# Optimization experiments

Measured on AMD Instinct MI355X. Metric: run time of the kernel, lower is better.

Reference implementation:

```python
import jax, jax.numpy as jnp
import numpy as np

B, T, D = 64, 512, 256   # batch, time, input feat
H = 256                  # LSTM hidden (features)


def setup_inputs() -> dict:
    key = jax.random.key(0)
    ks = jax.random.split(key, 16)
    s = lambda k, shp, fan: jax.random.normal(k, shp, jnp.float32) / np.sqrt(fan)
    return {
        "x":  jax.random.normal(ks[0], (B, T, D), jnp.float32),
        # LSTM params: fused gates order (i, f, g, o)
        "Wi": s(ks[1], (D, 4 * H), D),
        "Wh": s(ks[2], (H, 4 * H), H),
        "b":  jnp.zeros((4 * H,), jnp.float32),
        # single-head attention (head_dim = H)
        "Wq": s(ks[3], (H, H), H), "bq": jnp.zeros((H,), jnp.float32),
        "Wk": s(ks[4], (H, H), H), "bk": jnp.zeros((H,), jnp.float32),
        "Wv": s(ks[5], (H, H), H), "bv": jnp.zeros((H,), jnp.float32),
        "Wo": s(ks[6], (H, H), H), "bo": jnp.zeros((H,), jnp.float32),
        # MLP head
        "W1": s(ks[7], (H, 32), H), "b1": jnp.zeros((32,), jnp.float32),
        "W2": s(ks[8], (32, 3), 32), "b2": jnp.zeros((3,), jnp.float32),
    }


def _lstm_scan(x, Wi, Wh, b):
    # Precompute input-to-hidden projection for all timesteps (batched GEMM)
    xg = jnp.einsum('btd,dg->btg', x, Wi) + b          # [B,T,4H]
    c0 = jnp.zeros((x.shape[0], Wh.shape[0]), x.dtype)
    h0 = jnp.zeros_like(c0)

    def step(carry, xg_t):
        c, h = carry
        g = xg_t + h @ Wh                               # [B,4H]
        i, f, gg, o = jnp.split(g, 4, axis=-1)          # flax gate order i,f,g,o
        c = jax.nn.sigmoid(f) * c + jax.nn.sigmoid(i) * jnp.tanh(gg)
        h = jax.nn.sigmoid(o) * jnp.tanh(c)
        return (c, h), h

    (_, _), hs = jax.lax.scan(step, (c0, h0), jnp.swapaxes(xg, 0, 1))
    return jnp.swapaxes(hs, 0, 1)                       # [B,T,H]


def reference(x, Wi, Wh, b, Wq, bq, Wk, bk, Wv, bv, Wo, bo, W1, b1, W2, b2):
    h = _lstm_scan(x, Wi, Wh, b)                        # [B,T,H]
    # single-head dot-product attention (self-attention)
    q = h @ Wq + bq
    k = h @ Wk + bk
    v = h @ Wv + bv
    scale = 1.0 / np.sqrt(q.shape[-1]).astype(np.float32)
    scores = jnp.einsum('bqd,bkd->bqk', q * scale, k)   # [B,T,T]
    attn = jax.nn.softmax(scores, axis=-1)
    o = jnp.einsum('bqk,bkd->bqd', attn, v)
    o = o @ Wo + bo                                     # output projection
    # head on first timestep
    z = jax.nn.relu(o[:, 0, :] @ W1 + b1)
    return z @ W2 + b2                                  # [B,3]
```

## Files before the change

### kernel.cpp

```cpp
#include <hip/hip_runtime.h>
#include <hip/hip_bf16.h>


typedef __attribute__((ext_vector_type(8))) short short8;
typedef __attribute__((ext_vector_type(4))) float float4v;

__device__ __forceinline__ unsigned short f2bf(float f) {
  unsigned u = __builtin_bit_cast(unsigned, f);
  return (unsigned short)((u + 0x7fffu + ((u >> 16) & 1u)) >> 16);
}
__device__ __forceinline__ float bf2f(unsigned short h) {
  return __builtin_bit_cast(float, ((unsigned)h) << 16);
}
__device__ __forceinline__ float bcl(unsigned u) {
  return __builtin_bit_cast(float, u << 16);
}
__device__ __forceinline__ float bch(unsigned u) {
  return __builtin_bit_cast(float, u & 0xffff0000u);
}
__device__ __forceinline__ float sigm(float x) {
  return __builtin_amdgcn_rcpf(1.f + __expf(-x));
}
__device__ __forceinline__ float tanh_f(float x) {
  return 1.f - 2.f * __builtin_amdgcn_rcpf(1.f + __expf(2.f * x));
}

__global__ void prep_all(const float* __restrict__ x,
                         const float* __restrict__ Wi,
                         const float* __restrict__ Wh,
                         unsigned short* __restrict__ xbf,
                         unsigned short* __restrict__ WiT,
                         unsigned short* __restrict__ WhP) {
  const int bid = blockIdx.x, tid = threadIdx.x;
  if (bid < 8192) {
    size_t i = ((size_t)bid * 256 + tid) * 4;
    float4 v = *(const float4*)&x[i];
    unsigned long long pk = (unsigned long long)f2bf(v.x)
                          | ((unsigned long long)f2bf(v.y) << 16)
                          | ((unsigned long long)f2bf(v.z) << 32)
                          | ((unsigned long long)f2bf(v.w) << 48);
    *(unsigned long long*)&xbf[i] = pk;
  } else if (bid < 8448) {
    size_t i = ((size_t)(bid - 8192) * 256 + tid) * 4;
    float4 v = *(const float4*)&Wi[i];
    int k = (int)(i >> 10), n = (int)(i & 1023);
    WiT[(size_t)(n + 0) * 256 + k] = f2bf(v.x);
    WiT[(size_t)(n + 1) * 256 + k] = f2bf(v.y);
    WiT[(size_t)(n + 2) * 256 + k] = f2bf(v.z);
    WiT[(size_t)(n + 3) * 256 + k] = f2bf(v.w);
  } else {
    size_t i0 = ((size_t)(bid - 8448) * 256 + tid) * 4;
    int row = (int)(i0 >> 8);
    int colnat = (row & 3) * 256 + (row >> 7) * 32 + ((row >> 4) & 7) * 4 +
                 ((row >> 2) & 3);
    unsigned long long pk = 0;
#pragma unroll
    for (int j = 0; j < 4; ++j) {
      int k = (int)((i0 + j) & 255);
      pk |= (unsigned long long)f2bf(Wh[(size_t)k * 1024 + colnat]) << (16 * j);
    }
    *(unsigned long long*)&WhP[i0] = pk;
  }
}

#define XKP 40
__global__ __launch_bounds__(256) void xg_gemm(const unsigned short* __restrict__ xbf,
                                               const unsigned short* __restrict__ WiT,
                                               const float* __restrict__ bias,
                                               unsigned short* __restrict__ xg) {
  __shared__ unsigned short As[128 * XKP];
  __shared__ unsigned short Bs[128 * XKP];
  const int tid = threadIdx.x;
  const int n0 = blockIdx.x * 128, m0 = blockIdx.y * 128;
  const int wave = tid >> 6, lane = tid & 63, quad = lane >> 4, l16 = lane & 15;
  const int wm = wave >> 1, wn = wave & 1;

  float4v acc[4][4];
#pragma unroll
  for (int i = 0; i < 4; ++i)
#pragma unroll
    for (int j = 0; j < 4; ++j) acc[i][j] = (float4v){0.f, 0.f, 0.f, 0.f};

  const int rr = tid >> 2, c8 = (tid & 3) * 8;
  for (int k0 = 0; k0 < 256; k0 += 32) {
#pragma unroll
    for (int pp = 0; pp < 2; ++pp) {
      int r = pp * 64 + rr;
      *(uint4*)&As[r * XKP + c8] = *(const uint4*)&xbf[(size_t)(m0 + r) * 256 + k0 + c8];
      *(uint4*)&Bs[r * XKP + c8] = *(const uint4*)&WiT[(size_t)(n0 + r) * 256 + k0 + c8];
    }
    __syncthreads();
#pragma unroll
    for (int mt = 0; mt < 4; ++mt) {
      short8 af = *(const short8*)&As[(wm * 64 + mt * 16 + l16) * XKP + quad * 8];
#pragma unroll
      for (int nt = 0; nt < 4; ++nt) {
        short8 bf = *(const short8*)&Bs[(wn * 64 + nt * 16 + l16) * XKP + quad * 8];
        acc[mt][nt] = __builtin_amdgcn_mfma_f32_16x16x32_bf16(af, bf, acc[mt][nt], 0, 0, 0);
      }
    }
    __syncthreads();
  }
#pragma unroll
  for (int nt = 0; nt < 4; ++nt) {
    int col = n0 + wn * 64 + nt * 16 + l16;
    int gate = col >> 8, u = col & 255;
    float bv = bias[col];
#pragma unroll
    for (int mt = 0; mt < 4; ++mt) {
#pragma unroll
      for (int r = 0; r < 4; ++r) {
        int row = m0 + wm * 64 + mt * 16 + quad * 4 + r;
        int b = row >> 9, t = row & 511;
        xg[(((size_t)b * 512 + t) * 256 + u) * 4 + gate] = f2bf(acc[mt][nt][r] + bv);
      }
    }
  }
}

__global__ __launch_bounds__(512, 2) void lstm_scan(
    const unsigned short* __restrict__ WhP,
    const unsigned short* __restrict__ xg,
    unsigned short* __restrict__ hout) {
  __shared__ unsigned short WhL[16 * 4096];
  __shared__ unsigned short hA[2][256];
  const int tid = threadIdx.x;
  const int b = blockIdx.x;
  const int wave = tid >> 6, lane = tid & 63, quad = lane >> 4, l16 = lane & 15;

  short8 frA[3][8];
#pragma unroll
  for (int rt = 0; rt < 3; ++rt) {
    const unsigned short* src =
        WhP + ((size_t)wave * 128 + rt * 16 + l16) * 256 + quad * 8;
#pragma unroll
    for (int kt = 0; kt < 8; ++kt)
      frA[rt][kt] = *(const short8*)&src[kt * 32];
  }
#pragma unroll
  for (int i = 0; i < 16; ++i) {
    int rt = 3 + (i >> 3);
    int chunk = (i & 7) * 64 + lane;
    int rw = chunk >> 5, ch = chunk & 31;
    uint4 v = *(const uint4*)&WhP[((size_t)wave * 128 + rt * 16 + rw) * 256 + ch * 8];
    *(uint4*)((char*)WhL + (wave * 2 + rt - 3) * 8192 + rw * 512 +
              ((ch * 16) ^ ((rw & 7) << 4))) = v;
  }
  ((unsigned short*)hA)[tid] = 0;
  __syncthreads();

  const bool act = (l16 < 8);
  const int u = wave * 32 + l16 * 4 + quad;
  const unsigned short* xgp = xg + ((size_t)b * 512 * 256 + u) * 4;
  unsigned short* houtp = hout + (size_t)b * 512 * 256 + u;
  const char* ldsT = (const char*)WhL + wave * 2 * 8192 + l16 * 512;
  const unsigned short* sp5 = WhP + ((size_t)wave * 128 + 5 * 16 + l16) * 256 + quad * 8;
  const unsigned short* sp6 = WhP + ((size_t)wave * 128 + 6 * 16 + l16) * 256 + quad * 8;
  const unsigned short* sp7 = WhP + ((size_t)wave * 128 + 7 * 16 + l16) * 256 + quad * 8;
  float c = 0.f;

  for (int t = 0; t < 512; ++t) {
    short8 sb[8];
#pragma unroll
    for (int kt = 0; kt < 8; ++kt) sb[kt] = *(const short8*)&sp5[kt * 32];

    unsigned long long xv = 0;
    if (act) xv = *(const unsigned long long*)(xgp + (size_t)t * 1024);

    const char* hbuf = (const char*)hA[t & 1];
    short8 hb8[8];
#pragma unroll
    for (int kt = 0; kt < 8; ++kt)
      hb8[kt] = *(const short8*)(hbuf + kt * 64 + quad * 16);

    float4v g4 = (float4v){0.f, 0.f, 0.f, 0.f};

#pragma unroll
    for (int p = 0; p < 3; ++p) {
      float4v a = (float4v){0.f, 0.f, 0.f, 0.f};
#pragma unroll
      for (int kt = 0; kt < 8; ++kt)
        a = __builtin_amdgcn_mfma_f32_16x16x32_bf16(frA[p][kt], hb8[kt], a, 0, 0, 0);
      if (l16 == p) g4 = a;
    }

    short8 sc[8];
#pragma unroll
    for (int kt = 0; kt < 8; ++kt) sc[kt] = *(const short8*)&sp6[kt * 32];

#pragma unroll
    for (int p = 0; p < 2; ++p) {
      float4v a = (float4v){0.f, 0.f, 0.f, 0.f};
#pragma unroll
      for (int kt = 0; kt < 8; ++kt) {
        short8 al = *(const short8*)(ldsT + p * 8192 +
                                     ((kt * 64 + quad * 16) ^ ((l16 & 7) << 4)));
        a = __builtin_amdgcn_mfma_f32_16x16x32_bf16(al, hb8[kt], a, 0, 0, 0);
      }
      if (l16 == 3 + p) g4 = a;
    }

    {
      float4v a = (float4v){0.f, 0.f, 0.f, 0.f};
#pragma unroll
      for (int kt = 0; kt < 8; ++kt)
        a = __builtin_amdgcn_mfma_f32_16x16x32_bf16(sb[kt], hb8[kt], a, 0, 0, 0);
      if (l16 == 5) g4 = a;
    }
#pragma unroll
    for (int kt = 0; kt < 8; ++kt) sb[kt] = *(const short8*)&sp7[kt * 32];

    {
      float4v a = (float4v){0.f, 0.f, 0.f, 0.f};
#pragma unroll
      for (int kt = 0; kt < 8; ++kt)
        a = __builtin_amdgcn_mfma_f32_16x16x32_bf16(sc[kt], hb8[kt], a, 0, 0, 0);
      if (l16 == 6) g4 = a;
    }
    {
      float4v a = (float4v){0.f, 0.f, 0.f, 0.f};
#pragma unroll
      for (int kt = 0; kt < 8; ++kt)
        a = __builtin_amdgcn_mfma_f32_16x16x32_bf16(sb[kt], hb8[kt], a, 0, 0, 0);
      if (l16 == 7) g4 = a;
    }

    if (act) {
      float gi = g4[0] + bf2f((unsigned short)(xv));
      float gf = g4[1] + bf2f((unsigned short)(xv >> 16));
      float gG = g4[2] + bf2f((unsigned short)(xv >> 32));
      float go = g4[3] + bf2f((unsigned short)(xv >> 48));
      float cc = sigm(gf) * c + sigm(gi) * tanh_f(gG);
      c = cc;
      unsigned short h16 = f2bf(sigm(go) * tanh_f(cc));
      hA[(t + 1) & 1][u] = h16;
      houtp[(size_t)t * 256] = h16;
    }
    __syncthreads();
  }
}

__global__ __launch_bounds__(256) void attn_head(
    const unsigned short* __restrict__ hout,
    const float* __restrict__ Wq, const float* __restrict__ bq,
    const float* __restrict__ Wk, const float* __restrict__ bk,
    const float* __restrict__ Wv, const float* __restrict__ bv,
    const float* __restrict__ Wo, const float* __restrict__ bo,
    const float* __restrict__ W1, const float* __restrict__ b1,
    const float* __restrict__ W2, const float* __restrict__ b2,
    float* __restrict__ out) {
  __shared__ float h0S[256], q0S[256], red[256], usS[256], sS[512], hb4[4][256];
  __shared__ float oS[256], o1S[256], zS[32], cbS;
  const int b = blockIdx.x, tid = threadIdx.x, wave = tid >> 6, lane = tid & 63;
  const size_t hb_base = (size_t)b * 512 * 256;

  h0S[tid] = bf2f(hout[hb_base + tid]);
  __syncthreads();
  float a = 0.f;
  for (int k = 0; k < 256; ++k) a += h0S[k] * Wq[(size_t)k * 256 + tid];
  q0S[tid] = a + bq[tid];
  __syncthreads();
  red[tid] = q0S[tid] * bk[tid];
  __syncthreads();
  for (int s = 128; s > 0; s >>= 1) {
    if (tid < s) red[tid] += red[tid + s];
    __syncthreads();
  }
  if (tid == 0) cbS = 0.0625f * red[0];
  float acq = 0.f;
  const float* wr = &Wk[(size_t)tid * 256];
  for (int e = 0; e < 256; e += 4) {
    float4 w = *(const float4*)&wr[e];
    acq += w.x * q0S[e] + w.y * q0S[e + 1] + w.z * q0S[e + 2] + w.w * q0S[e + 3];
  }
  usS[tid] = 0.0625f * acq;
  __syncthreads();

  const float u0 = usS[lane * 4 + 0], u1 = usS[lane * 4 + 1];
  const float u2 = usS[lane * 4 + 2], u3 = usS[lane * 4 + 3];
  const float cbv = cbS;
  for (int i = 0; i < 128; ++i) {
    int t = i * 4 + wave;
    unsigned long long hv = *(const unsigned long long*)&hout[hb_base + (size_t)t * 256 + lane * 4];
    unsigned lo = (unsigned)hv, hi = (unsigned)(hv >> 32);
    float p = u0 * bcl(lo) + u1 * bch(lo) + u2 * bcl(hi) + u3 * bch(hi);
    for (int m = 1; m < 64; m <<= 1) p += __shfl_xor(p, m, 64);
    if (lane == 0) sS[t] = p + cbv;
  }
  __syncthreads();
  red[tid] = fmaxf(sS[tid], sS[tid + 256]);
  __syncthreads();
  for (int s = 128; s > 0; s >>= 1) {
    if (tid < s) red[tid] = fmaxf(red[tid], red[tid + s]);
    __syncthreads();
  }
  float mx = red[0];
  __syncthreads();
  float e0 = __expf(sS[tid] - mx), e1 = __expf(sS[tid + 256] - mx);
  sS[tid] = e0; sS[tid + 256] = e1;
  red[tid] = e0 + e1;
  __syncthreads();
  for (int s = 128; s > 0; s >>= 1) {
    if (tid < s) red[tid] += red[tid + s];
    __syncthreads();
  }
  float inv = 1.f / red[0];
  float a0 = 0.f, a1 = 0.f, a2 = 0.f, a3 = 0.f;
  const int d0 = lane * 4;
  for (int i = 0; i < 128; ++i) {
    int t = wave * 128 + i;
    float w = sS[t];
    unsigned long long hv = *(const unsigned long long*)&hout[hb_base + (size_t)t * 256 + d0];
    unsigned lo = (unsigned)hv, hi = (unsigned)(hv >> 32);
    a0 += w * bcl(lo); a1 += w * bch(lo); a2 += w * bcl(hi); a3 += w * bch(hi);
  }
  hb4[wave][d0] = a0; hb4[wave][d0 + 1] = a1; hb4[wave][d0 + 2] = a2; hb4[wave][d0 + 3] = a3;
  __syncthreads();
  h0S[tid] = (hb4[0][tid] + hb4[1][tid] + hb4[2][tid] + hb4[3][tid]) * inv;
  __syncthreads();

  a = 0.f;
  for (int k = 0; k < 256; ++k) a += h0S[k] * Wv[(size_t)k * 256 + tid];
  oS[tid] = a + bv[tid];
  __syncthreads();
  a = 0.f;
  for (int k = 0; k < 256; ++k) a += oS[k] * Wo[(size_t)k * 256 + tid];
  o1S[tid] = a + bo[tid];
  __syncthreads();
  if (tid < 32) {
    a = 0.f;
    for (int k = 0; k < 256; ++k) a += o1S[k] * W1[k * 32 + tid];
    zS[tid] = fmaxf(a + b1[tid], 0.f);
  }
  __syncthreads();
  if (tid < 3) {
    a = 0.f;
    for (int j = 0; j < 32; ++j) a += zS[j] * W2[j * 3 + tid];
    out[b * 3 + tid] = a + b2[tid];
  }
}

extern "C" void kernel_launch(void* const* d_in, const int* in_sizes, int n_in,
                              void* d_out, int out_size, void* d_ws, size_t ws_size,
                              hipStream_t stream) {
  const float* x  = (const float*)d_in[0];
  const float* Wi = (const float*)d_in[1];
  const float* Wh = (const float*)d_in[2];
  const float* bG = (const float*)d_in[3];
  const float* Wq = (const float*)d_in[4];
  const float* bq = (const float*)d_in[5];
  const float* Wk = (const float*)d_in[6];
  const float* bk = (const float*)d_in[7];
  const float* Wv = (const float*)d_in[8];
  const float* bv = (const float*)d_in[9];
  const float* Wo = (const float*)d_in[10];
  const float* bo = (const float*)d_in[11];
  const float* W1 = (const float*)d_in[12];
  const float* b1 = (const float*)d_in[13];
  const float* W2 = (const float*)d_in[14];
  const float* b2 = (const float*)d_in[15];
  float* out = (float*)d_out;
  char* ws = (char*)d_ws;

  unsigned short* xg   = (unsigned short*)(ws);
  unsigned short* hout = (unsigned short*)(ws + 67108864);
  unsigned short* xbf  = (unsigned short*)(ws + 83886080);
  unsigned short* WiT  = (unsigned short*)(ws + 100663296);
  unsigned short* WhP  = (unsigned short*)(ws + 101187584);

  prep_all<<<dim3(8704), dim3(256), 0, stream>>>(x, Wi, Wh, xbf, WiT, WhP);
  xg_gemm<<<dim3(8, 256), dim3(256), 0, stream>>>(xbf, WiT, bG, xg);
  lstm_scan<<<dim3(64), dim3(512), 0, stream>>>(WhP, xg, hout);
  attn_head<<<dim3(64), dim3(256), 0, stream>>>(hout, Wq, bq, Wk, bk, Wv, bv,
                                                Wo, bo, W1, b1, W2, b2, out);
}
```

Measured before the change: 1.161 ms.

## Rebalance LSTM Wh tiles across registers, LDS and streamed global loads per wave

Changes how the 8 per-wave 16-row tiles of the recurrent weight are split between resident registers (now 4), LDS (19 slots, 2-3 per wave) and per-step global reloads (1-2 per wave), with wave-dependent counts. The first streamed tile is prefetched at the end of the previous step so it overlaps the barrier. Occupancy is pinned via waves_per_eu. The goal is to cut per-timestep global/L2 traffic on the serial recurrence critical path. The cost is higher register pressure, a larger LDS footprint, and wave divergence in loop trip counts.

New measurement: 1.551 ms. 1.34x slower.

```diff
diff --git a/kernel.cpp b/kernel.cpp
--- a/kernel.cpp
+++ b/kernel.cpp
@@ -118,52 +118,57 @@
   }
 }
 
-__global__ __launch_bounds__(512, 2) void lstm_scan(
-    const unsigned short* __restrict__ WhP,
-    const unsigned short* __restrict__ xg,
-    unsigned short* __restrict__ hout) {
-  __shared__ unsigned short WhL[16 * 4096];
+__global__ __launch_bounds__(512)
+__attribute__((amdgpu_waves_per_eu(2, 2)))
+void lstm_scan(const unsigned short* __restrict__ WhP,
+               const unsigned short* __restrict__ xg,
+               unsigned short* __restrict__ hout) {
+  __shared__ unsigned short WhL[19 * 4096];
   __shared__ unsigned short hA[2][256];
   const int tid = threadIdx.x;
   const int b = blockIdx.x;
-  const int wave = tid >> 6, lane = tid & 63, quad = lane >> 4, l16 = lane & 15;
-
-  short8 frA[3][8];
-#pragma unroll
-  for (int rt = 0; rt < 3; ++rt) {
+  const int wave = __builtin_amdgcn_readfirstlane(tid >> 6);
+  const int lane = tid & 63, quad = lane >> 4, l16 = lane & 15;
+  const int nS = (wave < 3) ? 1 : 2;
+  const int nL = 4 - nS;
+  const int slotBase = (wave < 3) ? wave * 3 : 9 + (wave - 3) * 2;
+
+  short8 frA[4][8];
+#pragma unroll
+  for (int j = 0; j < 4; ++j) {
     const unsigned short* src =
-        WhP + ((size_t)wave * 128 + rt * 16 + l16) * 256 + quad * 8;
+        WhP + ((size_t)wave * 128 + (nS + j) * 16 + l16) * 256 + quad * 8;
 #pragma unroll
     for (int kt = 0; kt < 8; ++kt)
-      frA[rt][kt] = *(const short8*)&src[kt * 32];
-  }
-#pragma unroll
-  for (int i = 0; i < 16; ++i) {
-    int rt = 3 + (i >> 3);
-    int chunk = (i & 7) * 64 + lane;
-    int rw = chunk >> 5, ch = chunk & 31;
-    uint4 v = *(const uint4*)&WhP[((size_t)wave * 128 + rt * 16 + rw) * 256 + ch * 8];
-    *(uint4*)((char*)WhL + (wave * 2 + rt - 3) * 8192 + rw * 512 +
-              ((ch * 16) ^ ((rw & 7) << 4))) = v;
+      frA[j][kt] = *(const short8*)&src[kt * 32];
+  }
+  for (int j = 0; j < nL; ++j) {
+    int rt = nS + 4 + j;
+    for (int i = 0; i < 8; ++i) {
+      int chunk = i * 64 + lane;
+      int rw = chunk >> 5, ch = chunk & 31;
+      uint4 v = *(const uint4*)&WhP[((size_t)wave * 128 + rt * 16 + rw) * 256 + ch * 8];
+      *(uint4*)((char*)WhL + (slotBase + j) * 8192 + rw * 512 +
+                ((ch * 16) ^ ((rw & 7) << 4))) = v;
+    }
   }
   ((unsigned short*)hA)[tid] = 0;
-  __syncthreads();
 
   const bool act = (l16 < 8);
   const int u = wave * 32 + l16 * 4 + quad;
   const unsigned short* xgp = xg + ((size_t)b * 512 * 256 + u) * 4;
   unsigned short* houtp = hout + (size_t)b * 512 * 256 + u;
-  const char* ldsT = (const char*)WhL + wave * 2 * 8192 + l16 * 512;
-  const unsigned short* sp5 = WhP + ((size_t)wave * 128 + 5 * 16 + l16) * 256 + quad * 8;
-  const unsigned short* sp6 = WhP + ((size_t)wave * 128 + 6 * 16 + l16) * 256 + quad * 8;
-  const unsigned short* sp7 = WhP + ((size_t)wave * 128 + 7 * 16 + l16) * 256 + quad * 8;
+  const char* ldsT = (const char*)WhL + slotBase * 8192 + l16 * 512;
+  const unsigned short* sp0 = WhP + ((size_t)wave * 128 + 0 * 16 + l16) * 256 + quad * 8;
+  const unsigned short* sp1 = WhP + ((size_t)wave * 128 + 1 * 16 + l16) * 256 + quad * 8;
   float c = 0.f;
 
+  short8 sb[8];
+#pragma unroll
+  for (int kt = 0; kt < 8; ++kt) sb[kt] = *(const short8*)&sp0[kt * 32];
+  __syncthreads();
+
   for (int t = 0; t < 512; ++t) {
-    short8 sb[8];
-#pragma unroll
-    for (int kt = 0; kt < 8; ++kt) sb[kt] = *(const short8*)&sp5[kt * 32];
-
     unsigned long long xv = 0;
     if (act) xv = *(const unsigned long long*)(xgp + (size_t)t * 1024);
 
@@ -175,54 +180,39 @@
 
     float4v g4 = (float4v){0.f, 0.f, 0.f, 0.f};
 
-#pragma unroll
-    for (int p = 0; p < 3; ++p) {
+    {
       float4v a = (float4v){0.f, 0.f, 0.f, 0.f};
 #pragma unroll
       for (int kt = 0; kt < 8; ++kt)
-        a = __builtin_amdgcn_mfma_f32_16x16x32_bf16(frA[p][kt], hb8[kt], a, 0, 0, 0);
-      if (l16 == p) g4 = a;
-    }
-
-    short8 sc[8];
-#pragma unroll
-    for (int kt = 0; kt < 8; ++kt) sc[kt] = *(const short8*)&sp6[kt * 32];
-
-#pragma unroll
-    for (int p = 0; p < 2; ++p) {
+        a = __builtin_amdgcn_mfma_f32_16x16x32_bf16(sb[kt], hb8[kt], a, 0, 0, 0);
+      if (l16 == 0) g4 = a;
+    }
+    if (nS == 2) {
+#pragma unroll
+      for (int kt = 0; kt < 8; ++kt) sb[kt] = *(const short8*)&sp1[kt * 32];
       float4v a = (float4v){0.f, 0.f, 0.f, 0.f};
 #pragma unroll
+      for (int kt = 0; kt < 8; ++kt)
+        a = __builtin_amdgcn_mfma_f32_16x16x32_bf16(sb[kt], hb8[kt], a, 0, 0, 0);
+      if (l16 == 1) g4 = a;
+    }
+#pragma unroll
+    for (int j = 0; j < 4; ++j) {
+      float4v a = (float4v){0.f, 0.f, 0.f, 0.f};
+#pragma unroll
+      for (int kt = 0; kt < 8; ++kt)
+        a = __builtin_amdgcn_mfma_f32_16x16x32_bf16(frA[j][kt], hb8[kt], a, 0, 0, 0);
+      if (l16 == nS + j) g4 = a;
+    }
+    for (int j = 0; j < nL; ++j) {
+      float4v a = (float4v){0.f, 0.f, 0.f, 0.f};
+#pragma unroll
       for (int kt = 0; kt < 8; ++kt) {
-        short8 al = *(const short8*)(ldsT + p * 8192 +
+        short8 al = *(const short8*)(ldsT + j * 8192 +
                                      ((kt * 64 + quad * 16) ^ ((l16 & 7) << 4)));
         a = __builtin_amdgcn_mfma_f32_16x16x32_bf16(al, hb8[kt], a, 0, 0, 0);
       }
-      if (l16 == 3 + p) g4 = a;
-    }
-
-    {
-      float4v a = (float4v){0.f, 0.f, 0.f, 0.f};
-#pragma unroll
-      for (int kt = 0; kt < 8; ++kt)
-        a = __builtin_amdgcn_mfma_f32_16x16x32_bf16(sb[kt], hb8[kt], a, 0, 0, 0);
-      if (l16 == 5) g4 = a;
-    }
-#pragma unroll
-    for (int kt = 0; kt < 8; ++kt) sb[kt] = *(const short8*)&sp7[kt * 32];
-
-    {
-      float4v a = (float4v){0.f, 0.f, 0.f, 0.f};
-#pragma unroll
-      for (int kt = 0; kt < 8; ++kt)
-        a = __builtin_amdgcn_mfma_f32_16x16x32_bf16(sc[kt], hb8[kt], a, 0, 0, 0);
-      if (l16 == 6) g4 = a;
-    }
-    {
-      float4v a = (float4v){0.f, 0.f, 0.f, 0.f};
-#pragma unroll
-      for (int kt = 0; kt < 8; ++kt)
-        a = __builtin_amdgcn_mfma_f32_16x16x32_bf16(sb[kt], hb8[kt], a, 0, 0, 0);
-      if (l16 == 7) g4 = a;
+      if (l16 == nS + 4 + j) g4 = a;
     }
 
     if (act) {
@@ -236,6 +226,8 @@
       hA[(t + 1) & 1][u] = h16;
       houtp[(size_t)t * 256] = h16;
     }
+#pragma unroll
+    for (int kt = 0; kt < 8; ++kt) sb[kt] = *(const short8*)&sp0[kt * 32];
     __syncthreads();
   }
 }
```

## Stream Wh tiles from global through a rotating double-buffered register pipeline

Applied to the files above, without the earlier changes.

Stops keeping three Wh row tiles resident in registers. Six row tiles are now streamed from global/L2 every timestep through a two-slot register double buffer, each load issued one tile ahead of its use. LDS still holds two tiles, now tiles 6-7 instead of 3-4, and the launch-bounds minimum-blocks hint is dropped. This frees VGPRs and overlaps weight loads with MFMA work, but it adds more global loads on each serial recurrence step.

Measured after the change: 1.627 ms. 40.1% more time.

```diff
diff --git a/kernel.cpp b/kernel.cpp
--- a/kernel.cpp
+++ b/kernel.cpp
@@ -118,7 +118,7 @@
   }
 }
 
-__global__ __launch_bounds__(512, 2) void lstm_scan(
+__global__ __launch_bounds__(512) void lstm_scan(
     const unsigned short* __restrict__ WhP,
     const unsigned short* __restrict__ xg,
     unsigned short* __restrict__ hout) {
@@ -128,42 +128,33 @@
   const int b = blockIdx.x;
   const int wave = tid >> 6, lane = tid & 63, quad = lane >> 4, l16 = lane & 15;
 
-  short8 frA[3][8];
-#pragma unroll
-  for (int rt = 0; rt < 3; ++rt) {
-    const unsigned short* src =
-        WhP + ((size_t)wave * 128 + rt * 16 + l16) * 256 + quad * 8;
-#pragma unroll
-    for (int kt = 0; kt < 8; ++kt)
-      frA[rt][kt] = *(const short8*)&src[kt * 32];
-  }
 #pragma unroll
   for (int i = 0; i < 16; ++i) {
-    int rt = 3 + (i >> 3);
+    int rt = 6 + (i >> 3);
     int chunk = (i & 7) * 64 + lane;
     int rw = chunk >> 5, ch = chunk & 31;
     uint4 v = *(const uint4*)&WhP[((size_t)wave * 128 + rt * 16 + rw) * 256 + ch * 8];
-    *(uint4*)((char*)WhL + (wave * 2 + rt - 3) * 8192 + rw * 512 +
+    *(uint4*)((char*)WhL + (wave * 2 + rt - 6) * 8192 + rw * 512 +
               ((ch * 16) ^ ((rw & 7) << 4))) = v;
   }
   ((unsigned short*)hA)[tid] = 0;
-  __syncthreads();
 
   const bool act = (l16 < 8);
   const int u = wave * 32 + l16 * 4 + quad;
   const unsigned short* xgp = xg + ((size_t)b * 512 * 256 + u) * 4;
   unsigned short* houtp = hout + (size_t)b * 512 * 256 + u;
   const char* ldsT = (const char*)WhL + wave * 2 * 8192 + l16 * 512;
-  const unsigned short* sp5 = WhP + ((size_t)wave * 128 + 5 * 16 + l16) * 256 + quad * 8;
-  const unsigned short* sp6 = WhP + ((size_t)wave * 128 + 6 * 16 + l16) * 256 + quad * 8;
-  const unsigned short* sp7 = WhP + ((size_t)wave * 128 + 7 * 16 + l16) * 256 + quad * 8;
+  const unsigned short* sp = WhP + ((size_t)wave * 128 + l16) * 256 + quad * 8;
   float c = 0.f;
 
+  short8 buf[2][8];
+#pragma unroll
+  for (int kt = 0; kt < 8; ++kt) buf[0][kt] = *(const short8*)&sp[0 * 4096 + kt * 32];
+#pragma unroll
+  for (int kt = 0; kt < 8; ++kt) buf[1][kt] = *(const short8*)&sp[1 * 4096 + kt * 32];
+  __syncthreads();
+
   for (int t = 0; t < 512; ++t) {
-    short8 sb[8];
-#pragma unroll
-    for (int kt = 0; kt < 8; ++kt) sb[kt] = *(const short8*)&sp5[kt * 32];
-
     unsigned long long xv = 0;
     if (act) xv = *(const unsigned long long*)(xgp + (size_t)t * 1024);
 
@@ -176,17 +167,17 @@
     float4v g4 = (float4v){0.f, 0.f, 0.f, 0.f};
 
 #pragma unroll
-    for (int p = 0; p < 3; ++p) {
+    for (int p = 0; p < 6; ++p) {
       float4v a = (float4v){0.f, 0.f, 0.f, 0.f};
 #pragma unroll
       for (int kt = 0; kt < 8; ++kt)
-        a = __builtin_amdgcn_mfma_f32_16x16x32_bf16(frA[p][kt], hb8[kt], a, 0, 0, 0);
+        a = __builtin_amdgcn_mfma_f32_16x16x32_bf16(buf[p & 1][kt], hb8[kt], a, 0, 0, 0);
       if (l16 == p) g4 = a;
-    }
-
-    short8 sc[8];
-#pragma unroll
-    for (int kt = 0; kt < 8; ++kt) sc[kt] = *(const short8*)&sp6[kt * 32];
+      const int nrt = (p + 2) % 6;
+#pragma unroll
+      for (int kt = 0; kt < 8; ++kt)
+        buf[p & 1][kt] = *(const short8*)&sp[nrt * 4096 + kt * 32];
+    }
 
 #pragma unroll
     for (int p = 0; p < 2; ++p) {
@@ -197,32 +188,7 @@
                                      ((kt * 64 + quad * 16) ^ ((l16 & 7) << 4)));
         a = __builtin_amdgcn_mfma_f32_16x16x32_bf16(al, hb8[kt], a, 0, 0, 0);
       }
-      if (l16 == 3 + p) g4 = a;
-    }
-
-    {
-      float4v a = (float4v){0.f, 0.f, 0.f, 0.f};
-#pragma unroll
-      for (int kt = 0; kt < 8; ++kt)
-        a = __builtin_amdgcn_mfma_f32_16x16x32_bf16(sb[kt], hb8[kt], a, 0, 0, 0);
-      if (l16 == 5) g4 = a;
-    }
-#pragma unroll
-    for (int kt = 0; kt < 8; ++kt) sb[kt] = *(const short8*)&sp7[kt * 32];
-
-    {
-      float4v a = (float4v){0.f, 0.f, 0.f, 0.f};
-#pragma unroll
-      for (int kt = 0; kt < 8; ++kt)
-        a = __builtin_amdgcn_mfma_f32_16x16x32_bf16(sc[kt], hb8[kt], a, 0, 0, 0);
-      if (l16 == 6) g4 = a;
-    }
-    {
-      float4v a = (float4v){0.f, 0.f, 0.f, 0.f};
-#pragma unroll
-      for (int kt = 0; kt < 8; ++kt)
-        a = __builtin_amdgcn_mfma_f32_16x16x32_bf16(sb[kt], hb8[kt], a, 0, 0, 0);
-      if (l16 == 7) g4 = a;
+      if (l16 == 6 + p) g4 = a;
     }
 
     if (act) {
```
